# Kernel tuning notes

Measured on AMD Instinct MI355X. Metric: run time of the kernel, lower is better.

Reference implementation:

```python
import jax, jax.numpy as jnp
import numpy as np
from jax import lax


def _dtw_similarity_single(s1, s2):
    # s1: [L1, D], s2: [L2, D]  -- cosine distance matrix then min-plus DP
    s1n = s1 / jnp.linalg.norm(s1, axis=1, keepdims=True)
    s2n = s2 / jnp.linalg.norm(s2, axis=1, keepdims=True)
    dist = 1.0 - s1n @ s2n.T  # [L1, L2]

    L1, L2 = dist.shape
    first_row = jnp.cumsum(dist[0])  # dtw[0, :]

    def row_step(prev_row, dist_row):
        # prev_row: dtw[i-1, :]; dist_row: dist[i, :]
        first = prev_row[0] + dist_row[0]  # dtw[i, 0]

        def cell(left, x):
            d, up, up_diag = x
            val = d + jnp.minimum(jnp.minimum(up, left), up_diag)
            return val, val

        xs = (dist_row[1:], prev_row[1:], prev_row[:-1])
        _, rest = lax.scan(cell, first, xs)
        row = jnp.concatenate([first[None], rest])
        return row, None

    last_row, _ = lax.scan(row_step, first_row, dist[1:])
    dtw_distance = last_row[-1]
    normalized = dtw_distance / (L1 + L2)
    return 1.0 / (1.0 + normalized)


def setup_inputs() -> dict:
    key = jax.random.key(0)
    k1, k2 = jax.random.split(key)
    seq1 = jax.random.normal(k1, (64, 128, 1024), dtype=jnp.float32)
    seq2 = jax.random.normal(k2, (64, 256, 1024), dtype=jnp.float32)
    return {"seq1": seq1, "seq2": seq2}


def reference(seq1, seq2):
    # FastDTWEmbeddingSimilarity.forward: per-batch DTW similarity -> [batch]
    return jax.vmap(_dtw_similarity_single)(seq1, seq2)
```

## Files before the change

### kernel.cpp

```cpp
#include <hip/hip_runtime.h>
#include <cstddef>

#define L1n 128
#define L2n 256
#define Kn  1024

using frag_ab = __attribute__((ext_vector_type(8))) short;
using frag_cd = __attribute__((ext_vector_type(4))) float;

__device__ __forceinline__ unsigned pack_bf16(float x, float y) {
    unsigned ux = __float_as_uint(x);
    ux = (ux + 0x7FFFu + ((ux >> 16) & 1u)) >> 16;
    unsigned uy = __float_as_uint(y);
    uy = (uy + 0x7FFFu + ((uy >> 16) & 1u)) & 0xFFFF0000u;
    return ux | uy;
}

__global__ __launch_bounds__(256) void gemm_dist_kernel(
    const float* __restrict__ seq1,
    const float* __restrict__ seq2,
    float* __restrict__ dist)
{
    __shared__ __align__(16) unsigned char sA[2][8192];
    __shared__ __align__(16) unsigned char sB[2][8192];
    __shared__ float sInvA[64];
    __shared__ float sInvB[64];

    const int wg   = ((blockIdx.x & 7) << 6) + (blockIdx.x >> 3);
    const int b    = wg >> 3;
    const int mt   = (wg >> 2) & 1;
    const int nt   = wg & 3;
    const int t    = threadIdx.x;
    const int lane = t & 63;
    const int w    = t >> 6;
    const int wr   = w >> 1;
    const int wc   = w & 1;
    const int r    = t >> 2;
    const int j    = t & 3;
    const int swz  = (r & 7) << 4;

    const float4* pA = reinterpret_cast<const float4*>(
        seq1 + (size_t)b * (L1n * Kn) + (size_t)(mt * 64 + r) * Kn) + j;
    const float4* pB = reinterpret_cast<const float4*>(
        seq2 + (size_t)b * (L2n * Kn) + (size_t)(nt * 64 + r) * Kn) + j;

    float ssA = 0.0f, ssB = 0.0f;
    frag_cd acc[2][2] = {};

    float4 avA[4], bvA[4], avB[4], bvB[4];

    auto issue = [&](float4* av, float4* bv, int s) {
#pragma unroll
        for (int i = 0; i < 4; ++i) { av[i] = pA[s * 16 + 4 * i]; bv[i] = pB[s * 16 + 4 * i]; }
    };
    auto convert = [&](const float4* av, const float4* bv, int buf) {
#pragma unroll
        for (int i = 0; i < 4; ++i) {
            ssA += av[i].x * av[i].x + av[i].y * av[i].y + av[i].z * av[i].z + av[i].w * av[i].w;
            ssB += bv[i].x * bv[i].x + bv[i].y * bv[i].y + bv[i].z * bv[i].z + bv[i].w * bv[i].w;
            const int kb = (j + 4 * i) * 8;
            *reinterpret_cast<uint2*>(&sA[buf][r * 128 + (kb ^ swz)]) =
                make_uint2(pack_bf16(av[i].x, av[i].y), pack_bf16(av[i].z, av[i].w));
            *reinterpret_cast<uint2*>(&sB[buf][r * 128 + (kb ^ swz)]) =
                make_uint2(pack_bf16(bv[i].x, bv[i].y), pack_bf16(bv[i].z, bv[i].w));
        }
    };
    auto domfma = [&](int buf) {
#pragma unroll
        for (int kk = 0; kk < 2; ++kk) {
            const int kb = kk * 64 + ((lane >> 4) << 4);
            const int m0 = wr * 32 + (lane & 15);
            const int n0 = wc * 32 + (lane & 15);
            const int fswz = (lane & 7) << 4;
            frag_ab a0 = *reinterpret_cast<const frag_ab*>(&sA[buf][m0 * 128 + (kb ^ fswz)]);
            frag_ab a1 = *reinterpret_cast<const frag_ab*>(&sA[buf][(m0 + 16) * 128 + (kb ^ fswz)]);
            frag_ab b0 = *reinterpret_cast<const frag_ab*>(&sB[buf][n0 * 128 + (kb ^ fswz)]);
            frag_ab b1 = *reinterpret_cast<const frag_ab*>(&sB[buf][(n0 + 16) * 128 + (kb ^ fswz)]);
            acc[0][0] = __builtin_amdgcn_mfma_f32_16x16x32_bf16(b0, a0, acc[0][0], 0, 0, 0);
            acc[0][1] = __builtin_amdgcn_mfma_f32_16x16x32_bf16(b0, a1, acc[0][1], 0, 0, 0);
            acc[1][0] = __builtin_amdgcn_mfma_f32_16x16x32_bf16(b1, a0, acc[1][0], 0, 0, 0);
            acc[1][1] = __builtin_amdgcn_mfma_f32_16x16x32_bf16(b1, a1, acc[1][1], 0, 0, 0);
        }
    };

    issue(avA, bvA, 0);
    convert(avA, bvA, 0);
    issue(avA, bvA, 1);

#pragma unroll
    for (int s = 0; s < 16; s += 2) {
        __syncthreads();
        if (s + 2 < 16) issue(avB, bvB, s + 2);
        domfma(0);
        convert(avA, bvA, 1);

        __syncthreads();
        if (s + 3 < 16) issue(avA, bvA, s + 3);
        domfma(1);
        if (s + 2 < 16) convert(avB, bvB, 0);
    }

    ssA += __shfl_xor(ssA, 1); ssA += __shfl_xor(ssA, 2);
    ssB += __shfl_xor(ssB, 1); ssB += __shfl_xor(ssB, 2);
    if (j == 0) { sInvA[r] = rsqrtf(ssA); sInvB[r] = rsqrtf(ssB); }
    __syncthreads();

    float* dbase = dist + (size_t)b * (L1n * L2n);
#pragma unroll
    for (int nj = 0; nj < 2; ++nj)
#pragma unroll
        for (int mi = 0; mi < 2; ++mi) {
            const int m_l = wr * 32 + mi * 16 + (lane & 15);
            const int n_b = wc * 32 + nj * 16 + ((lane >> 4) << 2);
            const float ia = sInvA[m_l];
            const int grow = mt * 64 + m_l;
#pragma unroll
            for (int reg = 0; reg < 4; ++reg) {
                const int n_l = n_b + reg;
                dbase[(size_t)(nt * 64 + n_l) * L1n + grow] =
                    1.0f - acc[nj][mi][reg] * ia * sInvB[n_l];
            }
        }
}

__global__ __launch_bounds__(64) void dtw_kernel(
    const float* __restrict__ dist, float* __restrict__ out)
{
    const int b    = blockIdx.x;
    const int lane = threadIdx.x;
    const float INF = 3.0e38f;
    const bool lane0 = (lane == 0);
    const float* base = dist + (size_t)b * (L1n * L2n) + 2 * lane;

    float c0 = INF, c1 = INF;
    float sh0 = INF, sh1 = INF, sh2 = INF, sh3 = INF, sh4 = INF;

    auto ldval = [&](int tt) -> float2 {
        int jj = tt - 4 * lane;
        jj = jj < 0 ? 0 : (jj > L2n - 1 ? L2n - 1 : jj);
        return *reinterpret_cast<const float2*>(base + (size_t)jj * L1n);
    };

    auto step = [&](float2 d, bool t0) {
        float u = lane0 ? (t0 ? 0.0f : INF) : sh3;
        float g = lane0 ? INF : sh4;
        float ugm = fminf(u, g);
        float n0 = d.x + fminf(c0, ugm);
        float n1 = d.y + fminf(fminf(c1, c0), n0);
        float snew = __shfl_up(n1, 1);
        sh4 = sh3; sh3 = sh2; sh2 = sh1; sh1 = sh0; sh0 = snew;
        c0 = n0; c1 = n1;
    };

    float2 pfA[8], pfB[8];
#pragma unroll
    for (int u = 0; u < 8; ++u) pfA[u] = ldval(u);
#pragma unroll
    for (int u = 0; u < 8; ++u) pfB[u] = ldval(8 + u);

#pragma unroll
    for (int u = 0; u < 8; ++u) step(pfA[u], u == 0);
#pragma unroll
    for (int u = 0; u < 8; ++u) pfA[u] = ldval(16 + u);

    int t = 8;
    for (int i = 0; i < 31; ++i) {
        float2 curB[8];
#pragma unroll
        for (int u = 0; u < 8; ++u) curB[u] = pfB[u];
#pragma unroll
        for (int u = 0; u < 8; ++u) pfB[u] = ldval(t + 16 + u);
#pragma unroll
        for (int u = 0; u < 8; ++u) step(curB[u], false);

        float2 curA[8];
#pragma unroll
        for (int u = 0; u < 8; ++u) curA[u] = pfA[u];
#pragma unroll
        for (int u = 0; u < 8; ++u) pfA[u] = ldval(t + 24 + u);
#pragma unroll
        for (int u = 0; u < 8; ++u) step(curA[u], false);
        t += 16;
    }

#pragma unroll
    for (int u = 0; u < 4; ++u) step(pfB[u], false);

    if (lane == 63)
        out[b] = 1.0f / (1.0f + c1 * (1.0f / (float)(L1n + L2n)));
}

extern "C" void kernel_launch(void* const* d_in, const int* in_sizes, int n_in,
                              void* d_out, int out_size, void* d_ws, size_t ws_size,
                              hipStream_t stream) {
    const float* seq1 = (const float*)d_in[0];
    const float* seq2 = (const float*)d_in[1];
    float* out  = (float*)d_out;
    float* dist = (float*)d_ws;

    gemm_dist_kernel<<<dim3(512), dim3(256), 0, stream>>>(seq1, seq2, dist);
    dtw_kernel<<<dim3(64), dim3(64), 0, stream>>>(dist, out);
}
```

Measured before the change: 48.63 us.

## Enlarge GEMM tile to 128x128 with 512-thread blocks and single-buffer register staging

Each GEMM workgroup now computes a 128x128 tile of the distance matrix with 8 waves, where it used to compute 64x64 with 4 waves. This cuts redundant global reads of seq1 and seq2 rows across tiles and gives each wave more MFMA work per shared-memory fragment load. The K loop becomes a single rolled loop with one register staging buffer, and each thread loads contiguous float4s. The grid shrinks from 512 to 128 workgroups, which leaves many CUs idle on a large GPU and reduces how well loads overlap with compute.

```diff
diff --git a/kernel.cpp b/kernel.cpp
--- a/kernel.cpp
+++ b/kernel.cpp
@@ -4,6 +4,8 @@
 #define L1n 128
 #define L2n 256
 #define Kn  1024
+#define BK  64
+#define NSTEP (Kn / BK)
 
 using frag_ab = __attribute__((ext_vector_type(8))) short;
 using frag_cd = __attribute__((ext_vector_type(4))) float;
@@ -16,49 +18,49 @@
     return ux | uy;
 }
 
-__global__ __launch_bounds__(256) void gemm_dist_kernel(
+__global__ __launch_bounds__(512) void gemm_dist_kernel(
     const float* __restrict__ seq1,
     const float* __restrict__ seq2,
     float* __restrict__ dist)
 {
-    __shared__ __align__(16) unsigned char sA[2][8192];
-    __shared__ __align__(16) unsigned char sB[2][8192];
-    __shared__ float sInvA[64];
-    __shared__ float sInvB[64];
-
-    const int wg   = ((blockIdx.x & 7) << 6) + (blockIdx.x >> 3);
-    const int b    = wg >> 3;
-    const int mt   = (wg >> 2) & 1;
-    const int nt   = wg & 3;
+    __shared__ __align__(16) unsigned char sA[2][128 * 128];
+    __shared__ __align__(16) unsigned char sB[2][128 * 128];
+    __shared__ float sInvA[128];
+    __shared__ float sInvB[128];
+
+    const int wg   = ((blockIdx.x & 7) << 4) + (blockIdx.x >> 3);
+    const int b    = wg >> 1;
+    const int nt   = wg & 1;
     const int t    = threadIdx.x;
     const int lane = t & 63;
     const int w    = t >> 6;
-    const int wr   = w >> 1;
-    const int wc   = w & 1;
-    const int r    = t >> 2;
-    const int j    = t & 3;
-    const int swz  = (r & 7) << 4;
+    const int wr   = w >> 2;
+    const int wc   = w & 3;
+
+    const int r = t >> 2;
+    const int j = t & 3;
+    const int swz = (r & 7) << 4;
 
     const float4* pA = reinterpret_cast<const float4*>(
-        seq1 + (size_t)b * (L1n * Kn) + (size_t)(mt * 64 + r) * Kn) + j;
+        seq1 + (size_t)b * (L1n * Kn) + (size_t)r * Kn) + j * 4;
     const float4* pB = reinterpret_cast<const float4*>(
-        seq2 + (size_t)b * (L2n * Kn) + (size_t)(nt * 64 + r) * Kn) + j;
+        seq2 + (size_t)b * (L2n * Kn) + (size_t)(nt * 128 + r) * Kn) + j * 4;
 
     float ssA = 0.0f, ssB = 0.0f;
-    frag_cd acc[2][2] = {};
-
-    float4 avA[4], bvA[4], avB[4], bvB[4];
-
-    auto issue = [&](float4* av, float4* bv, int s) {
-#pragma unroll
-        for (int i = 0; i < 4; ++i) { av[i] = pA[s * 16 + 4 * i]; bv[i] = pB[s * 16 + 4 * i]; }
-    };
-    auto convert = [&](const float4* av, const float4* bv, int buf) {
+    frag_cd acc[2][4] = {};
+
+    float4 av[4], bv[4];
+
+    auto issue = [&](int s) {
+#pragma unroll
+        for (int i = 0; i < 4; ++i) { av[i] = pA[s * 16 + i]; bv[i] = pB[s * 16 + i]; }
+    };
+    auto convert = [&](int buf) {
 #pragma unroll
         for (int i = 0; i < 4; ++i) {
             ssA += av[i].x * av[i].x + av[i].y * av[i].y + av[i].z * av[i].z + av[i].w * av[i].w;
             ssB += bv[i].x * bv[i].x + bv[i].y * bv[i].y + bv[i].z * bv[i].z + bv[i].w * bv[i].w;
-            const int kb = (j + 4 * i) * 8;
+            const int kb = (j * 4 + i) * 8;
             *reinterpret_cast<uint2*>(&sA[buf][r * 128 + (kb ^ swz)]) =
                 make_uint2(pack_bf16(av[i].x, av[i].y), pack_bf16(av[i].z, av[i].w));
             *reinterpret_cast<uint2*>(&sB[buf][r * 128 + (kb ^ swz)]) =
@@ -69,35 +71,34 @@
 #pragma unroll
         for (int kk = 0; kk < 2; ++kk) {
             const int kb = kk * 64 + ((lane >> 4) << 4);
-            const int m0 = wr * 32 + (lane & 15);
-            const int n0 = wc * 32 + (lane & 15);
             const int fswz = (lane & 7) << 4;
-            frag_ab a0 = *reinterpret_cast<const frag_ab*>(&sA[buf][m0 * 128 + (kb ^ fswz)]);
-            frag_ab a1 = *reinterpret_cast<const frag_ab*>(&sA[buf][(m0 + 16) * 128 + (kb ^ fswz)]);
-            frag_ab b0 = *reinterpret_cast<const frag_ab*>(&sB[buf][n0 * 128 + (kb ^ fswz)]);
-            frag_ab b1 = *reinterpret_cast<const frag_ab*>(&sB[buf][(n0 + 16) * 128 + (kb ^ fswz)]);
+            const int ml = wr * 64 + (lane & 15);
+            const int nl = wc * 32 + (lane & 15);
+            frag_ab a0 = *reinterpret_cast<const frag_ab*>(&sA[buf][(ml +  0) * 128 + (kb ^ fswz)]);
+            frag_ab a1 = *reinterpret_cast<const frag_ab*>(&sA[buf][(ml + 16) * 128 + (kb ^ fswz)]);
+            frag_ab a2 = *reinterpret_cast<const frag_ab*>(&sA[buf][(ml + 32) * 128 + (kb ^ fswz)]);
+            frag_ab a3 = *reinterpret_cast<const frag_ab*>(&sA[buf][(ml + 48) * 128 + (kb ^ fswz)]);
+            frag_ab b0 = *reinterpret_cast<const frag_ab*>(&sB[buf][(nl +  0) * 128 + (kb ^ fswz)]);
+            frag_ab b1 = *reinterpret_cast<const frag_ab*>(&sB[buf][(nl + 16) * 128 + (kb ^ fswz)]);
             acc[0][0] = __builtin_amdgcn_mfma_f32_16x16x32_bf16(b0, a0, acc[0][0], 0, 0, 0);
             acc[0][1] = __builtin_amdgcn_mfma_f32_16x16x32_bf16(b0, a1, acc[0][1], 0, 0, 0);
+            acc[0][2] = __builtin_amdgcn_mfma_f32_16x16x32_bf16(b0, a2, acc[0][2], 0, 0, 0);
+            acc[0][3] = __builtin_amdgcn_mfma_f32_16x16x32_bf16(b0, a3, acc[0][3], 0, 0, 0);
             acc[1][0] = __builtin_amdgcn_mfma_f32_16x16x32_bf16(b1, a0, acc[1][0], 0, 0, 0);
             acc[1][1] = __builtin_amdgcn_mfma_f32_16x16x32_bf16(b1, a1, acc[1][1], 0, 0, 0);
+            acc[1][2] = __builtin_amdgcn_mfma_f32_16x16x32_bf16(b1, a2, acc[1][2], 0, 0, 0);
+            acc[1][3] = __builtin_amdgcn_mfma_f32_16x16x32_bf16(b1, a3, acc[1][3], 0, 0, 0);
         }
     };
 
-    issue(avA, bvA, 0);
-    convert(avA, bvA, 0);
-    issue(avA, bvA, 1);
-
-#pragma unroll
-    for (int s = 0; s < 16; s += 2) {
+    issue(0);
+    convert(0);
+
+    for (int s = 0; s < NSTEP; ++s) {
         __syncthreads();
-        if (s + 2 < 16) issue(avB, bvB, s + 2);
-        domfma(0);
-        convert(avA, bvA, 1);
-
-        __syncthreads();
-        if (s + 3 < 16) issue(avA, bvA, s + 3);
-        domfma(1);
-        if (s + 2 < 16) convert(avB, bvB, 0);
+        if (s + 1 < NSTEP) issue(s + 1);
+        domfma(s & 1);
+        if (s + 1 < NSTEP) convert((s + 1) & 1);
     }
 
     ssA += __shfl_xor(ssA, 1); ssA += __shfl_xor(ssA, 2);
@@ -109,15 +110,14 @@
 #pragma unroll
     for (int nj = 0; nj < 2; ++nj)
 #pragma unroll
-        for (int mi = 0; mi < 2; ++mi) {
-            const int m_l = wr * 32 + mi * 16 + (lane & 15);
+        for (int mi = 0; mi < 4; ++mi) {
+            const int m_l = wr * 64 + mi * 16 + (lane & 15);
             const int n_b = wc * 32 + nj * 16 + ((lane >> 4) << 2);
             const float ia = sInvA[m_l];
-            const int grow = mt * 64 + m_l;
 #pragma unroll
             for (int reg = 0; reg < 4; ++reg) {
                 const int n_l = n_b + reg;
-                dbase[(size_t)(nt * 64 + n_l) * L1n + grow] =
+                dbase[(size_t)(nt * 128 + n_l) * L1n + m_l] =
                     1.0f - acc[nj][mi][reg] * ia * sInvB[n_l];
             }
         }
@@ -198,6 +198,6 @@
     float* out  = (float*)d_out;
     float* dist = (float*)d_ws;
 
-    gemm_dist_kernel<<<dim3(512), dim3(256), 0, stream>>>(seq1, seq2, dist);
+    gemm_dist_kernel<<<dim3(128), dim3(512), 0, stream>>>(seq1, seq2, dist);
     dtw_kernel<<<dim3(64), dim3(64), 0, stream>>>(dist, out);
 }
```

Measured after the change: 63.62 us. +30.8%, slower.

## Stage fp32 tiles via direct global-to-LDS loads and convert to bf16 at fragment load

Applied to the files above, without the earlier changes.

The GEMM kernel now copies raw fp32 tiles straight from global memory into shared memory with global_load_lds, instead of loading into registers, converting to bf16 and writing LDS. Conversion to bf16 and the row sum-of-squares for normalization now happen when each wave reads its MFMA fragments, with norms reduced by cross-lane shuffles rather than through shared memory. This aims to cut register staging and VALU work in the load path and let copies overlap compute. In exchange the shared-memory footprint doubles, each fragment is converted by several waves, and the pipeline uses a rolled loop with one barrier per step.

```diff
diff --git a/kernel.cpp b/kernel.cpp
--- a/kernel.cpp
+++ b/kernel.cpp
@@ -4,9 +4,13 @@
 #define L1n 128
 #define L2n 256
 #define Kn  1024
+#define NSTEP 16
 
 using frag_ab = __attribute__((ext_vector_type(8))) short;
 using frag_cd = __attribute__((ext_vector_type(4))) float;
+
+typedef __attribute__((address_space(1))) const unsigned int gconst_u32;
+typedef __attribute__((address_space(3))) unsigned int lds_u32;
 
 __device__ __forceinline__ unsigned pack_bf16(float x, float y) {
     unsigned ux = __float_as_uint(x);
@@ -15,16 +19,25 @@
     uy = (uy + 0x7FFFu + ((uy >> 16) & 1u)) & 0xFFFF0000u;
     return ux | uy;
 }
+__device__ __forceinline__ float dot4(float4 v) {
+    return v.x * v.x + v.y * v.y + v.z * v.z + v.w * v.w;
+}
+__device__ __forceinline__ frag_ab mk_frag(float4 a, float4 b) {
+    union { frag_ab f; unsigned u[4]; } r;
+    r.u[0] = pack_bf16(a.x, a.y);
+    r.u[1] = pack_bf16(a.z, a.w);
+    r.u[2] = pack_bf16(b.x, b.y);
+    r.u[3] = pack_bf16(b.z, b.w);
+    return r.f;
+}
 
 __global__ __launch_bounds__(256) void gemm_dist_kernel(
     const float* __restrict__ seq1,
     const float* __restrict__ seq2,
     float* __restrict__ dist)
 {
-    __shared__ __align__(16) unsigned char sA[2][8192];
-    __shared__ __align__(16) unsigned char sB[2][8192];
-    __shared__ float sInvA[64];
-    __shared__ float sInvB[64];
+    __shared__ __align__(16) unsigned char sA[2][64 * 256];
+    __shared__ __align__(16) unsigned char sB[2][64 * 256];
 
     const int wg   = ((blockIdx.x & 7) << 6) + (blockIdx.x >> 3);
     const int b    = wg >> 3;
@@ -35,92 +48,105 @@
     const int w    = t >> 6;
     const int wr   = w >> 1;
     const int wc   = w & 1;
-    const int r    = t >> 2;
-    const int j    = t & 3;
-    const int swz  = (r & 7) << 4;
-
-    const float4* pA = reinterpret_cast<const float4*>(
-        seq1 + (size_t)b * (L1n * Kn) + (size_t)(mt * 64 + r) * Kn) + j;
-    const float4* pB = reinterpret_cast<const float4*>(
-        seq2 + (size_t)b * (L2n * Kn) + (size_t)(nt * 64 + r) * Kn) + j;
-
-    float ssA = 0.0f, ssB = 0.0f;
+
+    const int srow = t >> 4;
+    const int gswz = (srow & 7) << 4;
+    const int goff = ((t & 15) << 4) ^ gswz;
+    const char* gA = (const char*)seq1 +
+        ((size_t)b * L1n + mt * 64 + srow) * (Kn * 4) + goff;
+    const char* gB = (const char*)seq2 +
+        ((size_t)b * L2n + nt * 64 + srow) * (Kn * 4) + goff;
+    const int ldsw = w * 1024;
+
+    auto stage = [&](int s, int buf) {
+        const char* a = gA + (size_t)s * 256;
+        const char* p = gB + (size_t)s * 256;
+#pragma unroll
+        for (int i = 0; i < 4; ++i) {
+            __builtin_amdgcn_global_load_lds(
+                (gconst_u32*)(a + i * 65536),
+                (lds_u32*)(&sA[buf][i * 4096 + ldsw]), 16, 0, 0);
+            __builtin_amdgcn_global_load_lds(
+                (gconst_u32*)(p + i * 65536),
+                (lds_u32*)(&sB[buf][i * 4096 + ldsw]), 16, 0, 0);
+        }
+    };
+
     frag_cd acc[2][2] = {};
-
-    float4 avA[4], bvA[4], avB[4], bvB[4];
-
-    auto issue = [&](float4* av, float4* bv, int s) {
-#pragma unroll
-        for (int i = 0; i < 4; ++i) { av[i] = pA[s * 16 + 4 * i]; bv[i] = pB[s * 16 + 4 * i]; }
-    };
-    auto convert = [&](const float4* av, const float4* bv, int buf) {
-#pragma unroll
-        for (int i = 0; i < 4; ++i) {
-            ssA += av[i].x * av[i].x + av[i].y * av[i].y + av[i].z * av[i].z + av[i].w * av[i].w;
-            ssB += bv[i].x * bv[i].x + bv[i].y * bv[i].y + bv[i].z * bv[i].z + bv[i].w * bv[i].w;
-            const int kb = (j + 4 * i) * 8;
-            *reinterpret_cast<uint2*>(&sA[buf][r * 128 + (kb ^ swz)]) =
-                make_uint2(pack_bf16(av[i].x, av[i].y), pack_bf16(av[i].z, av[i].w));
-            *reinterpret_cast<uint2*>(&sB[buf][r * 128 + (kb ^ swz)]) =
-                make_uint2(pack_bf16(bv[i].x, bv[i].y), pack_bf16(bv[i].z, bv[i].w));
-        }
-    };
-    auto domfma = [&](int buf) {
+    float ssA[2] = {}, ssB[2] = {};
+    const int lswz = (lane & 7) << 4;
+    const int g32  = (lane >> 4) << 5;
+    const int rA0  = wr * 32 + (lane & 15);
+    const int rB0  = wc * 32 + (lane & 15);
+
+    auto consume = [&](int buf) {
+        frag_ab aF[2][2], bF[2][2];
 #pragma unroll
         for (int kk = 0; kk < 2; ++kk) {
-            const int kb = kk * 64 + ((lane >> 4) << 4);
-            const int m0 = wr * 32 + (lane & 15);
-            const int n0 = wc * 32 + (lane & 15);
-            const int fswz = (lane & 7) << 4;
-            frag_ab a0 = *reinterpret_cast<const frag_ab*>(&sA[buf][m0 * 128 + (kb ^ fswz)]);
-            frag_ab a1 = *reinterpret_cast<const frag_ab*>(&sA[buf][(m0 + 16) * 128 + (kb ^ fswz)]);
-            frag_ab b0 = *reinterpret_cast<const frag_ab*>(&sB[buf][n0 * 128 + (kb ^ fswz)]);
-            frag_ab b1 = *reinterpret_cast<const frag_ab*>(&sB[buf][(n0 + 16) * 128 + (kb ^ fswz)]);
-            acc[0][0] = __builtin_amdgcn_mfma_f32_16x16x32_bf16(b0, a0, acc[0][0], 0, 0, 0);
-            acc[0][1] = __builtin_amdgcn_mfma_f32_16x16x32_bf16(b0, a1, acc[0][1], 0, 0, 0);
-            acc[1][0] = __builtin_amdgcn_mfma_f32_16x16x32_bf16(b1, a0, acc[1][0], 0, 0, 0);
-            acc[1][1] = __builtin_amdgcn_mfma_f32_16x16x32_bf16(b1, a1, acc[1][1], 0, 0, 0);
-        }
-    };
-
-    issue(avA, bvA, 0);
-    convert(avA, bvA, 0);
-    issue(avA, bvA, 1);
-
-#pragma unroll
-    for (int s = 0; s < 16; s += 2) {
-        __syncthreads();
-        if (s + 2 < 16) issue(avB, bvB, s + 2);
-        domfma(0);
-        convert(avA, bvA, 1);
-
-        __syncthreads();
-        if (s + 3 < 16) issue(avA, bvA, s + 3);
-        domfma(1);
-        if (s + 2 < 16) convert(avB, bvB, 0);
-    }
-
-    ssA += __shfl_xor(ssA, 1); ssA += __shfl_xor(ssA, 2);
-    ssB += __shfl_xor(ssB, 1); ssB += __shfl_xor(ssB, 2);
-    if (j == 0) { sInvA[r] = rsqrtf(ssA); sInvB[r] = rsqrtf(ssB); }
-    __syncthreads();
-
-    float* dbase = dist + (size_t)b * (L1n * L2n);
-#pragma unroll
-    for (int nj = 0; nj < 2; ++nj)
-#pragma unroll
-        for (int mi = 0; mi < 2; ++mi) {
-            const int m_l = wr * 32 + mi * 16 + (lane & 15);
-            const int n_b = wc * 32 + nj * 16 + ((lane >> 4) << 2);
-            const float ia = sInvA[m_l];
-            const int grow = mt * 64 + m_l;
-#pragma unroll
-            for (int reg = 0; reg < 4; ++reg) {
-                const int n_l = n_b + reg;
-                dbase[(size_t)(nt * 64 + n_l) * L1n + grow] =
-                    1.0f - acc[nj][mi][reg] * ia * sInvB[n_l];
+            const int o0 = (kk * 128 + g32) ^ lswz;
+            const int o1 = (kk * 128 + g32 + 16) ^ lswz;
+#pragma unroll
+            for (int mi = 0; mi < 2; ++mi) {
+                const unsigned char* p = &sA[buf][(rA0 + mi * 16) * 256];
+                float4 lo = *reinterpret_cast<const float4*>(p + o0);
+                float4 hi = *reinterpret_cast<const float4*>(p + o1);
+                ssA[mi] += dot4(lo) + dot4(hi);
+                aF[mi][kk] = mk_frag(lo, hi);
+            }
+#pragma unroll
+            for (int nj = 0; nj < 2; ++nj) {
+                const unsigned char* p = &sB[buf][(rB0 + nj * 16) * 256];
+                float4 lo = *reinterpret_cast<const float4*>(p + o0);
+                float4 hi = *reinterpret_cast<const float4*>(p + o1);
+                ssB[nj] += dot4(lo) + dot4(hi);
+                bF[nj][kk] = mk_frag(lo, hi);
             }
         }
+#pragma unroll
+        for (int kk = 0; kk < 2; ++kk)
+#pragma unroll
+            for (int nj = 0; nj < 2; ++nj)
+#pragma unroll
+                for (int mi = 0; mi < 2; ++mi)
+                    acc[nj][mi] = __builtin_amdgcn_mfma_f32_16x16x32_bf16(
+                        bF[nj][kk], aF[mi][kk], acc[nj][mi], 0, 0, 0);
+    };
+
+    stage(0, 0);
+    for (int s = 0; s < NSTEP; ++s) {
+        __syncthreads();
+        if (s + 1 < NSTEP) stage(s + 1, (s + 1) & 1);
+        consume(s & 1);
+    }
+
+#pragma unroll
+    for (int i = 0; i < 2; ++i) {
+        ssA[i] += __shfl_xor(ssA[i], 16); ssA[i] += __shfl_xor(ssA[i], 32);
+        ssB[i] += __shfl_xor(ssB[i], 16); ssB[i] += __shfl_xor(ssB[i], 32);
+    }
+    const float iA0 = rsqrtf(ssA[0]), iA1 = rsqrtf(ssA[1]);
+    const float iB0 = rsqrtf(ssB[0]), iB1 = rsqrtf(ssB[1]);
+
+    float* dT = dist + (size_t)b * (L1n * L2n);
+    const int csub = (lane >> 4) << 2;
+#pragma unroll
+    for (int nj = 0; nj < 2; ++nj) {
+        const float ibn = (nj == 0) ? iB0 : iB1;  (void)ibn;
+        float ib[4];
+#pragma unroll
+        for (int x = 0; x < 4; ++x)
+            ib[x] = __shfl((nj == 0) ? iB0 : iB1, csub + x);
+#pragma unroll
+        for (int mi = 0; mi < 2; ++mi) {
+            const float ia = (mi == 0) ? iA0 : iA1;
+            const int row = mt * 64 + wr * 32 + mi * 16 + (lane & 15);
+            const int col = nt * 64 + wc * 32 + nj * 16 + csub;
+#pragma unroll
+            for (int x = 0; x < 4; ++x)
+                dT[(size_t)(col + x) * L1n + row] =
+                    1.0f - acc[nj][mi][x] * ia * ib[x];
+        }
+    }
 }
 
 __global__ __launch_bounds__(64) void dtw_kernel(
```

Measured after the change: 58.50 us. +20.3%, slower.
